# Kernel optimization log

Hardware: AMD Instinct MI355X
Metric: run time of the kernel (lower is better)

## Reference

```python
import jax, jax.numpy as jnp
import numpy as np

B, H, C = 1, 4, 32
D = H * C          # 128
S, L = 128, 256
EPS = 1e-5


def _axial_layer_norm(x, gamma, beta):
    # normalize over channel axis (axis=1) of [B, D, S, L]
    mu = jnp.mean(x, axis=1, keepdims=True)
    var = jnp.var(x, axis=1, keepdims=True)
    xn = (x - mu) * jax.lax.rsqrt(var + EPS)
    return xn * gamma[None, :, None, None] + beta[None, :, None, None]


def setup_inputs() -> dict:
    key = jax.random.key(0)
    ks = jax.random.split(key, 5)
    x = jax.random.normal(ks[0], (B, D, S, L), dtype=jnp.float32)
    w_row = jax.random.normal(ks[1], (3 * D, D), dtype=jnp.float32) * 0.02
    b_row = jax.random.normal(ks[2], (3 * D,), dtype=jnp.float32) * 0.02
    w_col = jax.random.normal(ks[3], (3 * D, D), dtype=jnp.float32) * 0.02
    b_col = jax.random.normal(ks[4], (3 * D,), dtype=jnp.float32) * 0.02
    return {
        "x": x,
        "w_row": w_row, "b_row": b_row,
        "w_col": w_col, "b_col": b_col,
        "gamma1": jnp.ones((D,), jnp.float32), "beta1": jnp.zeros((D,), jnp.float32),
        "gamma2": jnp.ones((D,), jnp.float32), "beta2": jnp.zeros((D,), jnp.float32),
    }


def _qkv(x, w, b):
    # 1x1 conv == channel matmul: [3D, D] x [B, D, S, L] -> [B, 3D, S, L]
    qkv = jnp.einsum('od,bdsl->bosl', w, x) + b[None, :, None, None]
    q, k, v = jnp.split(qkv, 3, axis=1)
    rs = lambda t: t.reshape(t.shape[0], H, C, S, L)
    return rs(q), rs(k), rs(v)


def reference(x, w_row, b_row, w_col, b_col, gamma1, beta1, gamma2, beta2):
    # --- row attention (attend along L within each row s) ---
    q, k, v = _qkv(x, w_row, b_row)
    row_attn = jnp.einsum('bhcsi,bhcsj->bhsij', q, k)   # [B,H,S,L,L], no 1/sqrt(d) scaling (as in source)
    row_attn = jax.nn.softmax(row_attn, axis=-1)
    row_out = jnp.einsum('bhsij,bhdsj->bhdsi', row_attn, v).reshape(x.shape[0], D, S, L)
    out = _axial_layer_norm(x + row_out, gamma1, beta1)

    # --- column attention (attend along S within each column l) ---
    q, k, v = _qkv(out, w_col, b_col)
    col_attn = jnp.einsum('bhcil,bhcjl->bhijl', q, k)   # [B,H,S,S,L]
    col_attn = jax.nn.softmax(col_attn, axis=-2)
    col_out = jnp.einsum('bhijl,bhdjl->bhdil', col_attn, v).reshape(x.shape[0], D, S, L)
    out = _axial_layer_norm(out + col_out, gamma2, beta2)
    return out
```

## Files before the change

### kernel.cpp

```cpp
#include <hip/hip_runtime.h>
#include <hip/hip_bf16.h>

#define SL     32768
#define EPS_LN 1e-5f

typedef unsigned short u16;
typedef __attribute__((ext_vector_type(8))) short bf16x8;
typedef __attribute__((ext_vector_type(4))) float f32x4;

#define MFMA16(a, b, c) __builtin_amdgcn_mfma_f32_16x16x32_bf16((a), (b), (c), 0, 0, 0)

__device__ inline u16 f2bf(float f) {
    __hip_bfloat16 h = __float2bfloat16(f);
    return *reinterpret_cast<u16*>(&h);
}
__device__ inline float bf2f(u16 u) {
    unsigned v = ((unsigned)u) << 16;
    float f;
    __builtin_memcpy(&f, &v, 4);
    return f;
}
__device__ inline uint4 pack8(float4 a, float4 b) {
    union { uint4 v; u16 u[8]; } U;
    U.u[0] = f2bf(a.x); U.u[1] = f2bf(a.y); U.u[2] = f2bf(a.z); U.u[3] = f2bf(a.w);
    U.u[4] = f2bf(b.x); U.u[5] = f2bf(b.y); U.u[6] = f2bf(b.z); U.u[7] = f2bf(b.w);
    return U.v;
}

__global__ __launch_bounds__(256) void wcast_kernel(const float* __restrict__ wr,
                                                    const float* __restrict__ wc,
                                                    u16* __restrict__ wrb,
                                                    u16* __restrict__ wcb) {
    const int i = blockIdx.x * 256 + threadIdx.x;
    const int NW = 384 * 128 / 8;
    const float* src = (i < NW) ? wr : wc;
    u16* dst = (i < NW) ? wrb : wcb;
    const int j = (i < NW) ? i : i - NW;
    float4 a = ((const float4*)src)[j * 2];
    float4 b = ((const float4*)src)[j * 2 + 1];
    ((uint4*)dst)[j] = pack8(a, b);
}

__global__ __launch_bounds__(512) void qkv_mfma(const float* __restrict__ in,
                                                const u16* __restrict__ wb,
                                                const float* __restrict__ bq,
                                                u16* __restrict__ qT,
                                                u16* __restrict__ kT,
                                                u16* __restrict__ vb) {
    __shared__ u16 xT[64][136];
    __shared__ float bs[384];
    const int n0 = blockIdx.x * 64;
    const int t = threadIdx.x;
    const int lane = t & 63, wv = t >> 6, lo = lane & 15, hi = lane >> 4;

    if (t < 384) bs[t] = bq[t];

    #pragma unroll
    for (int itr = 0; itr < 2; ++itr) {
        const int u = t + itr * 512;
        const int d = u & 127, noct = u >> 7;
        const float* src = in + (size_t)d * SL + n0 + noct * 8;
        float4 f0 = *(const float4*)src;
        float4 f1 = *(const float4*)(src + 4);
        xT[noct * 8 + 0][d] = f2bf(f0.x);
        xT[noct * 8 + 1][d] = f2bf(f0.y);
        xT[noct * 8 + 2][d] = f2bf(f0.z);
        xT[noct * 8 + 3][d] = f2bf(f0.w);
        xT[noct * 8 + 4][d] = f2bf(f1.x);
        xT[noct * 8 + 5][d] = f2bf(f1.y);
        xT[noct * 8 + 6][d] = f2bf(f1.z);
        xT[noct * 8 + 7][d] = f2bf(f1.w);
    }
    __syncthreads();

    bf16x8 af[3][4];
    #pragma unroll
    for (int om = 0; om < 3; ++om)
        #pragma unroll
        for (int ks = 0; ks < 4; ++ks)
            af[om][ks] = *(const bf16x8*)(wb + (size_t)(wv * 48 + om * 16 + lo) * 128
                                             + hi * 8 + ks * 32);

    #pragma unroll
    for (int nt = 0; nt < 4; ++nt) {
        const int n = n0 + nt * 16 + lo;
        bf16x8 bfr[4];
        #pragma unroll
        for (int ks = 0; ks < 4; ++ks)
            bfr[ks] = *(const bf16x8*)&xT[nt * 16 + lo][hi * 8 + ks * 32];
        #pragma unroll
        for (int om = 0; om < 3; ++om) {
            const int obase = wv * 48 + om * 16;
            f32x4 acc = {0.f, 0.f, 0.f, 0.f};
            #pragma unroll
            for (int ks = 0; ks < 4; ++ks)
                acc = MFMA16(af[om][ks], bfr[ks], acc);
            if (obase < 256) {
                u16* tbuf = (obase < 128) ? qT : kT;
                const int ob = obase & 127;
                const int h = ob >> 5;
                const int cb = (ob & 31) + hi * 4;
                ushort4 o4;
                o4.x = f2bf(acc[0] + bs[obase + hi * 4 + 0]);
                o4.y = f2bf(acc[1] + bs[obase + hi * 4 + 1]);
                o4.z = f2bf(acc[2] + bs[obase + hi * 4 + 2]);
                o4.w = f2bf(acc[3] + bs[obase + hi * 4 + 3]);
                *(ushort4*)(tbuf + (size_t)h * SL * 32 + (size_t)n * 32 + cb) = o4;
            } else {
                const int orow = obase - 256 + hi * 4;
                #pragma unroll
                for (int r = 0; r < 4; ++r)
                    vb[(size_t)(orow + r) * SL + n] = f2bf(acc[r] + bs[obase + hi * 4 + r]);
            }
        }
    }
}

template<int KLEN, int NTHR>
__global__ __launch_bounds__(NTHR) void attn_kernel(const u16* __restrict__ qT,
                                                    const u16* __restrict__ kT,
                                                    const u16* __restrict__ vb,
                                                    u16* __restrict__ ao) {
    constexpr int NJT = KLEN / 16;
    constexpr int NW = NTHR / 64;
    constexpr int NOUT = SL / KLEN;
    __shared__ u16 PT[NW][2][16][36];

    const int bid = blockIdx.x;
    const int outer = bid % NOUT;
    const int h = bid / NOUT;
    const int base = outer * KLEN;
    const int t = threadIdx.x;
    const int lane = t & 63, wv = t >> 6, lo = lane & 15, hi = lane >> 4;
    const int i0w = wv * 32;

    const u16* qh = qT + (size_t)h * SL * 32;
    const u16* kh = kT + (size_t)h * SL * 32;
    const u16* vh = vb + (size_t)h * 32 * SL;

    bf16x8 qf0 = *(const bf16x8*)(qh + (size_t)(base + i0w + lo) * 32 + hi * 8);
    bf16x8 qf1 = *(const bf16x8*)(qh + (size_t)(base + i0w + 16 + lo) * 32 + hi * 8);

    f32x4 o00 = {0.f, 0.f, 0.f, 0.f}, o01 = {0.f, 0.f, 0.f, 0.f};
    f32x4 o10 = {0.f, 0.f, 0.f, 0.f}, o11 = {0.f, 0.f, 0.f, 0.f};
    float ls0[4] = {0.f, 0.f, 0.f, 0.f};
    float ls1[4] = {0.f, 0.f, 0.f, 0.f};

    #pragma unroll
    for (int jt = 0; jt < NJT; ++jt) {
        bf16x8 kf = *(const bf16x8*)(kh + (size_t)(base + jt * 16 + lo) * 32 + hi * 8);
        f32x4 z = {0.f, 0.f, 0.f, 0.f};
        f32x4 s0 = MFMA16(qf0, kf, z);
        f32x4 s1 = MFMA16(qf1, kf, z);
        #pragma unroll
        for (int r = 0; r < 4; ++r) {
            float p0 = __expf(s0[r]);
            ls0[r] += p0;
            PT[wv][0][hi * 4 + r][(jt & 1) * 16 + lo] = f2bf(p0);
            float p1 = __expf(s1[r]);
            ls1[r] += p1;
            PT[wv][1][hi * 4 + r][(jt & 1) * 16 + lo] = f2bf(p1);
        }
        if (jt & 1) {
            const int jb = (jt - 1) * 16;
            bf16x8 pf0 = *(const bf16x8*)&PT[wv][0][lo][hi * 8];
            bf16x8 pf1 = *(const bf16x8*)&PT[wv][1][lo][hi * 8];
            bf16x8 v0 = *(const bf16x8*)(vh + (size_t)lo * SL + base + jb + hi * 8);
            bf16x8 v1 = *(const bf16x8*)(vh + (size_t)(16 + lo) * SL + base + jb + hi * 8);
            o00 = MFMA16(pf0, v0, o00);
            o01 = MFMA16(pf0, v1, o01);
            o10 = MFMA16(pf1, v0, o10);
            o11 = MFMA16(pf1, v1, o11);
        }
    }
    #pragma unroll
    for (int r = 0; r < 4; ++r) {
        float v0 = ls0[r];
        v0 += __shfl_xor(v0, 1);
        v0 += __shfl_xor(v0, 2);
        v0 += __shfl_xor(v0, 4);
        v0 += __shfl_xor(v0, 8);
        ls0[r] = 1.f / v0;
        float v1 = ls1[r];
        v1 += __shfl_xor(v1, 1);
        v1 += __shfl_xor(v1, 2);
        v1 += __shfl_xor(v1, 4);
        v1 += __shfl_xor(v1, 8);
        ls1[r] = 1.f / v1;
    }
    {
        ushort4 o4;
        o4.x = f2bf(o00[0] * ls0[0]);
        o4.y = f2bf(o00[1] * ls0[1]);
        o4.z = f2bf(o00[2] * ls0[2]);
        o4.w = f2bf(o00[3] * ls0[3]);
        *(ushort4*)(ao + (size_t)(h * 32 + lo) * SL + base + i0w + hi * 4) = o4;
        o4.x = f2bf(o01[0] * ls0[0]);
        o4.y = f2bf(o01[1] * ls0[1]);
        o4.z = f2bf(o01[2] * ls0[2]);
        o4.w = f2bf(o01[3] * ls0[3]);
        *(ushort4*)(ao + (size_t)(h * 32 + 16 + lo) * SL + base + i0w + hi * 4) = o4;
        o4.x = f2bf(o10[0] * ls1[0]);
        o4.y = f2bf(o10[1] * ls1[1]);
        o4.z = f2bf(o10[2] * ls1[2]);
        o4.w = f2bf(o10[3] * ls1[3]);
        *(ushort4*)(ao + (size_t)(h * 32 + lo) * SL + base + i0w + 16 + hi * 4) = o4;
        o4.x = f2bf(o11[0] * ls1[0]);
        o4.y = f2bf(o11[1] * ls1[1]);
        o4.z = f2bf(o11[2] * ls1[2]);
        o4.w = f2bf(o11[3] * ls1[3]);
        *(ushort4*)(ao + (size_t)(h * 32 + 16 + lo) * SL + base + i0w + 16 + hi * 4) = o4;
    }
}

__global__ __launch_bounds__(512) void qkv_attn2(const u16* __restrict__ in,
                                                 const u16* __restrict__ wb,
                                                 const float* __restrict__ bq,
                                                 u16* __restrict__ ao) {
    __shared__ u16 xS[128][136];
    __shared__ u16 qkS[2][4][128][36];
    __shared__ u16 vS[4][32][136];
    __shared__ u16 PT[8][2][16][36];
    __shared__ float bs[384];

    const int l = blockIdx.x;
    const size_t p0 = (size_t)l * 128;
    const int t = threadIdx.x;
    const int lane = t & 63, wv = t >> 6, lo = lane & 15, hi = lane >> 4;

    if (t < 384) bs[t] = bq[t];
    #pragma unroll
    for (int itr = 0; itr < 4; ++itr) {
        const int u = t + itr * 512;
        const int n = u >> 4, seg = u & 15;
        *(uint4*)&xS[n][seg * 8] = *(const uint4*)(in + (p0 + n) * 128 + seg * 8);
    }
    __syncthreads();

    bf16x8 af[3][4];
    #pragma unroll
    for (int om = 0; om < 3; ++om)
        #pragma unroll
        for (int ks = 0; ks < 4; ++ks)
            af[om][ks] = *(const bf16x8*)(wb + (size_t)(wv * 48 + om * 16 + lo) * 128
                                             + hi * 8 + ks * 32);
    #pragma unroll
    for (int nt = 0; nt < 8; ++nt) {
        const int n = nt * 16 + lo;
        bf16x8 bfr[4];
        #pragma unroll
        for (int ks = 0; ks < 4; ++ks)
            bfr[ks] = *(const bf16x8*)&xS[n][hi * 8 + ks * 32];
        #pragma unroll
        for (int om = 0; om < 3; ++om) {
            const int obase = wv * 48 + om * 16;
            f32x4 acc = {0.f, 0.f, 0.f, 0.f};
            #pragma unroll
            for (int ks = 0; ks < 4; ++ks)
                acc = MFMA16(af[om][ks], bfr[ks], acc);
            if (obase < 256) {
                const int qk = obase >> 7;
                const int ob = obase & 127;
                const int h = ob >> 5;
                const int cb = (ob & 31) + hi * 4;
                ushort4 o4;
                o4.x = f2bf(acc[0] + bs[obase + hi * 4 + 0]);
                o4.y = f2bf(acc[1] + bs[obase + hi * 4 + 1]);
                o4.z = f2bf(acc[2] + bs[obase + hi * 4 + 2]);
                o4.w = f2bf(acc[3] + bs[obase + hi * 4 + 3]);
                *(ushort4*)&qkS[qk][h][n][cb] = o4;
            } else {
                const int vr = obase - 256 + hi * 4;
                #pragma unroll
                for (int r = 0; r < 4; ++r) {
                    const int o = vr + r;
                    vS[o >> 5][o & 31][n] = f2bf(acc[r] + bs[obase + hi * 4 + r]);
                }
            }
        }
    }
    __syncthreads();

    const int h = wv >> 1;
    u16 (*oS)[136] = xS;

    #pragma unroll
    for (int g = 0; g < 2; ++g) {
        const int ib = (wv & 1) * 64 + g * 32;
        bf16x8 qf0 = *(const bf16x8*)&qkS[0][h][ib + lo][hi * 8];
        bf16x8 qf1 = *(const bf16x8*)&qkS[0][h][ib + 16 + lo][hi * 8];

        f32x4 o00 = {0.f, 0.f, 0.f, 0.f}, o01 = {0.f, 0.f, 0.f, 0.f};
        f32x4 o10 = {0.f, 0.f, 0.f, 0.f}, o11 = {0.f, 0.f, 0.f, 0.f};
        float ls0[4] = {0.f, 0.f, 0.f, 0.f};
        float ls1[4] = {0.f, 0.f, 0.f, 0.f};

        #pragma unroll
        for (int jt = 0; jt < 8; ++jt) {
            bf16x8 kf = *(const bf16x8*)&qkS[1][h][jt * 16 + lo][hi * 8];
            f32x4 z = {0.f, 0.f, 0.f, 0.f};
            f32x4 s0 = MFMA16(qf0, kf, z);
            f32x4 s1 = MFMA16(qf1, kf, z);
            #pragma unroll
            for (int r = 0; r < 4; ++r) {
                float pv0 = __expf(s0[r]);
                ls0[r] += pv0;
                PT[wv][0][hi * 4 + r][(jt & 1) * 16 + lo] = f2bf(pv0);
                float pv1 = __expf(s1[r]);
                ls1[r] += pv1;
                PT[wv][1][hi * 4 + r][(jt & 1) * 16 + lo] = f2bf(pv1);
            }
            if (jt & 1) {
                const int jb = (jt - 1) * 16;
                bf16x8 pf0 = *(const bf16x8*)&PT[wv][0][lo][hi * 8];
                bf16x8 pf1 = *(const bf16x8*)&PT[wv][1][lo][hi * 8];
                bf16x8 v0 = *(const bf16x8*)&vS[h][lo][jb + hi * 8];
                bf16x8 v1 = *(const bf16x8*)&vS[h][16 + lo][jb + hi * 8];
                o00 = MFMA16(pf0, v0, o00);
                o01 = MFMA16(pf0, v1, o01);
                o10 = MFMA16(pf1, v0, o10);
                o11 = MFMA16(pf1, v1, o11);
            }
        }
        #pragma unroll
        for (int r = 0; r < 4; ++r) {
            float v0 = ls0[r];
            v0 += __shfl_xor(v0, 1);
            v0 += __shfl_xor(v0, 2);
            v0 += __shfl_xor(v0, 4);
            v0 += __shfl_xor(v0, 8);
            ls0[r] = 1.f / v0;
            float v1 = ls1[r];
            v1 += __shfl_xor(v1, 1);
            v1 += __shfl_xor(v1, 2);
            v1 += __shfl_xor(v1, 4);
            v1 += __shfl_xor(v1, 8);
            ls1[r] = 1.f / v1;
        }
        #pragma unroll
        for (int r = 0; r < 4; ++r) {
            oS[h * 32 + lo][ib + hi * 4 + r]           = f2bf(o00[r] * ls0[r]);
            oS[h * 32 + 16 + lo][ib + hi * 4 + r]      = f2bf(o01[r] * ls0[r]);
            oS[h * 32 + lo][ib + 16 + hi * 4 + r]      = f2bf(o10[r] * ls1[r]);
            oS[h * 32 + 16 + lo][ib + 16 + hi * 4 + r] = f2bf(o11[r] * ls1[r]);
        }
    }
    __syncthreads();

    #pragma unroll
    for (int itr = 0; itr < 4; ++itr) {
        const int u = t + itr * 512;
        const int ch = u >> 4, seg = u & 15;
        *(uint4*)(ao + (size_t)ch * SL + p0 + seg * 8) = *(const uint4*)&oS[ch][seg * 8];
    }
}

__global__ __launch_bounds__(256) void ln_mid(const float* __restrict__ in0,
                                              const u16* __restrict__ in1,
                                              const float* __restrict__ g,
                                              const float* __restrict__ be,
                                              u16* __restrict__ outp) {
    __shared__ float val[128][69];
    __shared__ float redS[4][72];
    __shared__ float redQ[4][72];
    __shared__ float stat[64][2];
    __shared__ float gs[128], bes[128];
    const int bid = blockIdx.x;
    const int r0 = (bid / 16) * 4;
    const int c0 = (bid % 16) * 16;
    const int t = threadIdx.x;
    const int pos = t & 63, q = t >> 6;
    const size_t gp = (size_t)(r0 + (pos >> 4)) * 256 + c0 + (pos & 15);

    if (t < 128) { gs[t] = g[t]; bes[t] = be[t]; }
    float s = 0.f, ss = 0.f;
    #pragma unroll 4
    for (int dd = 0; dd < 32; ++dd) {
        const int d = q * 32 + dd;
        float v = in0[(size_t)d * SL + gp] + bf2f(in1[(size_t)d * SL + gp]);
        val[d][pos] = v;
        s += v; ss += v * v;
    }
    redS[q][pos] = s;
    redQ[q][pos] = ss;
    __syncthreads();
    if (t < 64) {
        const float S  = redS[0][t] + redS[1][t] + redS[2][t] + redS[3][t];
        const float SS = redQ[0][t] + redQ[1][t] + redQ[2][t] + redQ[3][t];
        const float mean = S * (1.f / 128.f);
        const float var  = SS * (1.f / 128.f) - mean * mean;
        stat[t][0] = mean;
        stat[t][1] = rsqrtf(var + EPS_LN);
    }
    __syncthreads();

    {
        const int pr = pos >> 4, pc = pos & 15;
        const size_t pp = (size_t)(c0 + pc) * 128 + r0 + pr;
        const float mean = stat[pos][0], rstd = stat[pos][1];
        union { uint4 v[4]; u16 u[32]; } O;
        #pragma unroll
        for (int dd = 0; dd < 32; ++dd) {
            const int d = q * 32 + dd;
            O.u[dd] = f2bf((val[d][pos] - mean) * rstd * gs[d] + bes[d]);
        }
        uint4* dst = (uint4*)(outp + pp * 128 + q * 32);
        #pragma unroll
        for (int k = 0; k < 4; ++k) dst[k] = O.v[k];
    }
}

__global__ __launch_bounds__(256) void ln_out(const u16* __restrict__ in0,
                                              const u16* __restrict__ in1,
                                              const float* __restrict__ g,
                                              const float* __restrict__ be,
                                              float* __restrict__ outp) {
    __shared__ float val[128][69];
    __shared__ float redS[4][72];
    __shared__ float redQ[4][72];
    __shared__ float stat[64][2];
    const int bid = blockIdx.x;
    const int r0 = (bid / 8) * 4;
    const int c0 = (bid % 8) * 16;
    const int t = threadIdx.x;
    const int pos = t & 63, q = t >> 6;
    const size_t gp = (size_t)(r0 + (pos >> 4)) * 128 + c0 + (pos & 15);

    float s = 0.f, ss = 0.f;
    {
        union { uint4 v[4]; u16 u[32]; } A;
        const uint4* src = (const uint4*)(in0 + gp * 128 + q * 32);
        #pragma unroll
        for (int k = 0; k < 4; ++k) A.v[k] = src[k];
        #pragma unroll 4
        for (int dd = 0; dd < 32; ++dd) {
            const int d = q * 32 + dd;
            float v = bf2f(A.u[dd]) + bf2f(in1[(size_t)d * SL + gp]);
            val[d][pos] = v;
            s += v; ss += v * v;
        }
    }
    redS[q][pos] = s;
    redQ[q][pos] = ss;
    __syncthreads();
    if (t < 64) {
        const float S  = redS[0][t] + redS[1][t] + redS[2][t] + redS[3][t];
        const float SS = redQ[0][t] + redQ[1][t] + redQ[2][t] + redQ[3][t];
        const float mean = S * (1.f / 128.f);
        const float var  = SS * (1.f / 128.f) - mean * mean;
        stat[t][0] = mean;
        stat[t][1] = rsqrtf(var + EPS_LN);
    }
    __syncthreads();

    {
        const int d = t >> 1;
        const int ch = (t & 1) * 8;
        const float gd = g[d], bd = be[d];
        #pragma unroll
        for (int cc = 0; cc < 8; ++cc) {
            const int c = ch + cc;
            float ov[4];
            #pragma unroll
            for (int r = 0; r < 4; ++r) {
                const int p = r * 16 + c;
                ov[r] = (val[d][p] - stat[p][0]) * stat[p][1] * gd + bd;
            }
            float* dst = outp + (size_t)d * SL + (c0 + c) * 256 + r0;
            *(float4*)dst = make_float4(ov[0], ov[1], ov[2], ov[3]);
        }
    }
}

extern "C" void kernel_launch(void* const* d_in, const int* in_sizes, int n_in,
                              void* d_out, int out_size, void* d_ws, size_t ws_size,
                              hipStream_t stream) {
    const float* x     = (const float*)d_in[0];
    const float* w_row = (const float*)d_in[1];
    const float* b_row = (const float*)d_in[2];
    const float* w_col = (const float*)d_in[3];
    const float* b_col = (const float*)d_in[4];
    const float* g1    = (const float*)d_in[5];
    const float* be1   = (const float*)d_in[6];
    const float* g2    = (const float*)d_in[7];
    const float* be2   = (const float*)d_in[8];
    float* out = (float*)d_out;

    char* base = (char*)d_ws;
    u16* qTb = (u16*)base;                        base += (size_t)128 * SL * 2;
    u16* kTb = (u16*)base;                        base += (size_t)128 * SL * 2;
    u16* vbb = (u16*)base;                        base += (size_t)128 * SL * 2;
    u16* ao16 = (u16*)base;                       base += (size_t)128 * SL * 2;
    u16* o1b  = (u16*)base;                       base += (size_t)128 * SL * 2;
    u16* wrb  = (u16*)base;                       base += (size_t)384 * 128 * 2;
    u16* wcb  = (u16*)base;

    wcast_kernel<<<48, 256, 0, stream>>>(w_row, w_col, wrb, wcb);
    qkv_mfma<<<512, 512, 0, stream>>>(x, wrb, b_row, qTb, kTb, vbb);
    attn_kernel<256, 512><<<512, 512, 0, stream>>>(qTb, kTb, vbb, ao16);
    ln_mid<<<512, 256, 0, stream>>>(x, ao16, g1, be1, o1b);
    qkv_attn2<<<256, 512, 0, stream>>>(o1b, wcb, b_col, ao16);
    ln_out<<<512, 256, 0, stream>>>(o1b, ao16, g2, be2, out);
}
```

Baseline: 91.56 us.

## Split column-attention kernel per head to launch more smaller blocks

```diff
diff --git a/kernel.cpp b/kernel.cpp
--- a/kernel.cpp
+++ b/kernel.cpp
@@ -213,37 +213,36 @@
     }
 }
 
-__global__ __launch_bounds__(512) void qkv_attn2(const u16* __restrict__ in,
+__global__ __launch_bounds__(384) void qkv_attn2(const u16* __restrict__ in,
                                                  const u16* __restrict__ wb,
                                                  const float* __restrict__ bq,
                                                  u16* __restrict__ ao) {
     __shared__ u16 xS[128][136];
-    __shared__ u16 qkS[2][4][128][36];
-    __shared__ u16 vS[4][32][136];
-    __shared__ u16 PT[8][2][16][36];
-    __shared__ float bs[384];
-
-    const int l = blockIdx.x;
+    __shared__ u16 qkS[2][128][36];
+    __shared__ u16 vS[32][136];
+    __shared__ u16 PT[4][2][16][36];
+    __shared__ float bs[96];
+
+    const int bid = blockIdx.x;
+    const int l = bid >> 2;
+    const int h = bid & 3;
     const size_t p0 = (size_t)l * 128;
     const int t = threadIdx.x;
     const int lane = t & 63, wv = t >> 6, lo = lane & 15, hi = lane >> 4;
 
-    if (t < 384) bs[t] = bq[t];
-    #pragma unroll
-    for (int itr = 0; itr < 4; ++itr) {
-        const int u = t + itr * 512;
-        const int n = u >> 4, seg = u & 15;
+    if (t < 96) bs[t] = bq[(t >> 5) * 128 + h * 32 + (t & 31)];
+    for (int idx = t; idx < 2048; idx += 384) {
+        const int n = idx >> 4, seg = idx & 15;
         *(uint4*)&xS[n][seg * 8] = *(const uint4*)(in + (p0 + n) * 128 + seg * 8);
     }
-    __syncthreads();
-
-    bf16x8 af[3][4];
-    #pragma unroll
-    for (int om = 0; om < 3; ++om)
-        #pragma unroll
-        for (int ks = 0; ks < 4; ++ks)
-            af[om][ks] = *(const bf16x8*)(wb + (size_t)(wv * 48 + om * 16 + lo) * 128
-                                             + hi * 8 + ks * 32);
+
+    const int grow = (wv >> 1) * 128 + h * 32 + (wv & 1) * 16 + lo;
+    bf16x8 af[4];
+    #pragma unroll
+    for (int ks = 0; ks < 4; ++ks)
+        af[ks] = *(const bf16x8*)(wb + (size_t)grow * 128 + hi * 8 + ks * 32);
+    __syncthreads();
+
     #pragma unroll
     for (int nt = 0; nt < 8; ++nt) {
         const int n = nt * 16 + lo;
@@ -251,44 +250,31 @@
         #pragma unroll
         for (int ks = 0; ks < 4; ++ks)
             bfr[ks] = *(const bf16x8*)&xS[n][hi * 8 + ks * 32];
-        #pragma unroll
-        for (int om = 0; om < 3; ++om) {
-            const int obase = wv * 48 + om * 16;
-            f32x4 acc = {0.f, 0.f, 0.f, 0.f};
+        f32x4 acc = {0.f, 0.f, 0.f, 0.f};
+        #pragma unroll
+        for (int ks = 0; ks < 4; ++ks)
+            acc = MFMA16(af[ks], bfr[ks], acc);
+        const int jb = wv * 16 + hi * 4;
+        if (wv < 4) {
+            ushort4 o4;
+            o4.x = f2bf(acc[0] + bs[jb + 0]);
+            o4.y = f2bf(acc[1] + bs[jb + 1]);
+            o4.z = f2bf(acc[2] + bs[jb + 2]);
+            o4.w = f2bf(acc[3] + bs[jb + 3]);
+            *(ushort4*)&qkS[wv >> 1][n][(wv & 1) * 16 + hi * 4] = o4;
+        } else {
             #pragma unroll
-            for (int ks = 0; ks < 4; ++ks)
-                acc = MFMA16(af[om][ks], bfr[ks], acc);
-            if (obase < 256) {
-                const int qk = obase >> 7;
-                const int ob = obase & 127;
-                const int h = ob >> 5;
-                const int cb = (ob & 31) + hi * 4;
-                ushort4 o4;
-                o4.x = f2bf(acc[0] + bs[obase + hi * 4 + 0]);
-                o4.y = f2bf(acc[1] + bs[obase + hi * 4 + 1]);
-                o4.z = f2bf(acc[2] + bs[obase + hi * 4 + 2]);
-                o4.w = f2bf(acc[3] + bs[obase + hi * 4 + 3]);
-                *(ushort4*)&qkS[qk][h][n][cb] = o4;
-            } else {
-                const int vr = obase - 256 + hi * 4;
-                #pragma unroll
-                for (int r = 0; r < 4; ++r) {
-                    const int o = vr + r;
-                    vS[o >> 5][o & 31][n] = f2bf(acc[r] + bs[obase + hi * 4 + r]);
-                }
-            }
-        }
-    }
-    __syncthreads();
-
-    const int h = wv >> 1;
+            for (int r = 0; r < 4; ++r)
+                vS[(wv & 1) * 16 + hi * 4 + r][n] = f2bf(acc[r] + bs[jb + r]);
+        }
+    }
+    __syncthreads();
+
     u16 (*oS)[136] = xS;
-
-    #pragma unroll
-    for (int g = 0; g < 2; ++g) {
-        const int ib = (wv & 1) * 64 + g * 32;
-        bf16x8 qf0 = *(const bf16x8*)&qkS[0][h][ib + lo][hi * 8];
-        bf16x8 qf1 = *(const bf16x8*)&qkS[0][h][ib + 16 + lo][hi * 8];
+    if (wv < 4) {
+        const int i0w = wv * 32;
+        bf16x8 qf0 = *(const bf16x8*)&qkS[0][i0w + lo][hi * 8];
+        bf16x8 qf1 = *(const bf16x8*)&qkS[0][i0w + 16 + lo][hi * 8];
 
         f32x4 o00 = {0.f, 0.f, 0.f, 0.f}, o01 = {0.f, 0.f, 0.f, 0.f};
         f32x4 o10 = {0.f, 0.f, 0.f, 0.f}, o11 = {0.f, 0.f, 0.f, 0.f};
@@ -297,7 +283,7 @@
 
         #pragma unroll
         for (int jt = 0; jt < 8; ++jt) {
-            bf16x8 kf = *(const bf16x8*)&qkS[1][h][jt * 16 + lo][hi * 8];
+            bf16x8 kf = *(const bf16x8*)&qkS[1][jt * 16 + lo][hi * 8];
             f32x4 z = {0.f, 0.f, 0.f, 0.f};
             f32x4 s0 = MFMA16(qf0, kf, z);
             f32x4 s1 = MFMA16(qf1, kf, z);
@@ -311,11 +297,11 @@
                 PT[wv][1][hi * 4 + r][(jt & 1) * 16 + lo] = f2bf(pv1);
             }
             if (jt & 1) {
-                const int jb = (jt - 1) * 16;
+                const int jb2 = (jt - 1) * 16;
                 bf16x8 pf0 = *(const bf16x8*)&PT[wv][0][lo][hi * 8];
                 bf16x8 pf1 = *(const bf16x8*)&PT[wv][1][lo][hi * 8];
-                bf16x8 v0 = *(const bf16x8*)&vS[h][lo][jb + hi * 8];
-                bf16x8 v1 = *(const bf16x8*)&vS[h][16 + lo][jb + hi * 8];
+                bf16x8 v0 = *(const bf16x8*)&vS[lo][jb2 + hi * 8];
+                bf16x8 v1 = *(const bf16x8*)&vS[16 + lo][jb2 + hi * 8];
                 o00 = MFMA16(pf0, v0, o00);
                 o01 = MFMA16(pf0, v1, o01);
                 o10 = MFMA16(pf1, v0, o10);
@@ -339,19 +325,18 @@
         }
         #pragma unroll
         for (int r = 0; r < 4; ++r) {
-            oS[h * 32 + lo][ib + hi * 4 + r]           = f2bf(o00[r] * ls0[r]);
-            oS[h * 32 + 16 + lo][ib + hi * 4 + r]      = f2bf(o01[r] * ls0[r]);
-            oS[h * 32 + lo][ib + 16 + hi * 4 + r]      = f2bf(o10[r] * ls1[r]);
-            oS[h * 32 + 16 + lo][ib + 16 + hi * 4 + r] = f2bf(o11[r] * ls1[r]);
-        }
-    }
-    __syncthreads();
-
-    #pragma unroll
-    for (int itr = 0; itr < 4; ++itr) {
-        const int u = t + itr * 512;
-        const int ch = u >> 4, seg = u & 15;
-        *(uint4*)(ao + (size_t)ch * SL + p0 + seg * 8) = *(const uint4*)&oS[ch][seg * 8];
+            oS[lo][i0w + hi * 4 + r]           = f2bf(o00[r] * ls0[r]);
+            oS[16 + lo][i0w + hi * 4 + r]      = f2bf(o01[r] * ls0[r]);
+            oS[lo][i0w + 16 + hi * 4 + r]      = f2bf(o10[r] * ls1[r]);
+            oS[16 + lo][i0w + 16 + hi * 4 + r] = f2bf(o11[r] * ls1[r]);
+        }
+    }
+    __syncthreads();
+
+    for (int idx = t; idx < 512; idx += 384) {
+        const int ch = idx >> 4, seg = idx & 15;
+        *(uint4*)(ao + (size_t)(h * 32 + ch) * SL + p0 + seg * 8) =
+            *(const uint4*)&oS[ch][seg * 8];
     }
 }
 
@@ -499,6 +484,6 @@
     qkv_mfma<<<512, 512, 0, stream>>>(x, wrb, b_row, qTb, kTb, vbb);
     attn_kernel<256, 512><<<512, 512, 0, stream>>>(qTb, kTb, vbb, ao16);
     ln_mid<<<512, 256, 0, stream>>>(x, ao16, g1, be1, o1b);
-    qkv_attn2<<<256, 512, 0, stream>>>(o1b, wcb, b_col, ao16);
+    qkv_attn2<<<1024, 384, 0, stream>>>(o1b, wcb, b_col, ao16);
     ln_out<<<512, 256, 0, stream>>>(o1b, ao16, g2, be2, out);
 }
```

Result: slower. 100.5 us (+9.7%).
